# Kernel optimization log

Measured on AMD Instinct MI355X. Metric: run time of the kernel, lower is better.

Reference implementation:

```python
import jax, jax.numpy as jnp
import numpy as np

B, S, E, H = 4, 2048, 1024, 16
D = E // H  # d_k = 64
NEG = -1000000000.0  # matches torch masked_fill constant


def setup_inputs() -> dict:
    rk = jax.random.key(0)
    kq, kk, kv, km = jax.random.split(rk, 4)
    query = jax.random.normal(kq, (B, S, E), dtype=jnp.float32)
    key = jax.random.normal(kk, (B, S, E), dtype=jnp.float32)
    value = jax.random.normal(kv, (B, S, E), dtype=jnp.float32)
    mask = jax.random.randint(km, (B, S, S), 0, 2, dtype=jnp.int32)
    return {"query": query, "key": key, "value": value, "mask": mask}


def _split_heads(x):
    # (B, S, E) -> (B, H, S, D)
    return x.reshape(B, S, H, D).transpose(0, 2, 1, 3)


def reference(query, key, value, mask):
    q = _split_heads(query)
    k = _split_heads(key)
    v = _split_heads(value)
    scale = np.float32(1.0 / np.sqrt(D))
    scores = jnp.einsum('bhqd,bhkd->bhqk', q, k) * scale  # (B,H,S,S)
    scores = jnp.where(mask[:, None, :, :] == 0, jnp.float32(NEG), scores)
    weights = jax.nn.softmax(scores, axis=-1)
    attn = jnp.einsum('bhqk,bhkd->bhqd', weights, v)  # (B,H,S,D)
    concat = attn.transpose(0, 2, 1, 3).reshape(B, S, E)
    return concat
```

## Files before the change

kernel.cpp:

```cpp
#include <hip/hip_runtime.h>
#include <hip/hip_bf16.h>
#include <math.h>

constexpr int B = 4, S = 2048, E = 1024, H = 16, D = 64;
constexpr float NEGF = -1000000000.0f;

typedef __attribute__((ext_vector_type(8))) short short8;
typedef __attribute__((ext_vector_type(16))) float f32x16;

__device__ inline short f2bf(float x) {
    __hip_bfloat16 h = __float2bfloat16(x);
    return *reinterpret_cast<short*>(&h);
}
__device__ inline unsigned pk(float a, float b) {
    return (unsigned)(unsigned short)f2bf(a) | ((unsigned)(unsigned short)f2bf(b) << 16);
}
__device__ inline void gl_lds16(const void* g, void* l) {
    __builtin_amdgcn_global_load_lds(
        (const __attribute__((address_space(1))) unsigned int*)g,
        (__attribute__((address_space(3))) unsigned int*)l, 16, 0, 0);
}

constexpr size_t WS_Q  = 0;
constexpr size_t WS_K  = 18874368;
constexpr size_t WS_VT = 37748736;
constexpr size_t WS_MB = 56623104;
constexpr size_t WS_NEED = 58720256;

__global__ void cvt_qk(const float* __restrict__ src, char* __restrict__ dst, float scale) {
    int g = blockIdx.x * 256 + threadIdx.x;
    int rowd = g >> 2, qtr = g & 3;
    int b = rowd >> 15, h = (rowd >> 11) & 15, s = rowd & 2047;
    const float* p = src + ((size_t)(b * S + s)) * E + h * 64 + qtr * 16;
    float4 v0 = *(const float4*)(p + 0),  v1 = *(const float4*)(p + 4);
    float4 v2 = *(const float4*)(p + 8),  v3 = *(const float4*)(p + 12);
    uint4 o0, o1;
    o0.x = pk(v0.x * scale, v0.y * scale); o0.y = pk(v0.z * scale, v0.w * scale);
    o0.z = pk(v1.x * scale, v1.y * scale); o0.w = pk(v1.z * scale, v1.w * scale);
    o1.x = pk(v2.x * scale, v2.y * scale); o1.y = pk(v2.z * scale, v2.w * scale);
    o1.z = pk(v3.x * scale, v3.y * scale); o1.w = pk(v3.z * scale, v3.w * scale);
    char* d = dst + (size_t)rowd * 144 + qtr * 32;
    *(uint4*)d = o0; *(uint4*)(d + 16) = o1;
}

__global__ void vtrans(const float* __restrict__ V, char* __restrict__ dst) {
    __shared__ float Vf[64][69];
    int t = threadIdx.x;
    int bh = blockIdx.x >> 5, kt = blockIdx.x & 31;
    int b = bh >> 4, h = bh & 15;
    {
        int r = t >> 2, c4 = (t & 3) * 16;
        const float* p = V + ((size_t)(b * S + kt * 64 + r)) * E + h * 64 + c4;
        float4 a = *(const float4*)(p + 0), bb = *(const float4*)(p + 4);
        float4 c = *(const float4*)(p + 8), dd = *(const float4*)(p + 12);
        *(float4*)&Vf[r][c4 + 0] = a;  *(float4*)&Vf[r][c4 + 4] = bb;
        *(float4*)&Vf[r][c4 + 8] = c;  *(float4*)&Vf[r][c4 + 12] = dd;
    }
    __syncthreads();
    int d = t >> 2, sq = (t & 3) * 16;
    float v[16];
#pragma unroll
    for (int i = 0; i < 16; ++i) v[i] = Vf[sq + i][d];
    uint4 o0, o1;
    o0.x = pk(v[0], v[1]);  o0.y = pk(v[2], v[3]);
    o0.z = pk(v[4], v[5]);  o0.w = pk(v[6], v[7]);
    o1.x = pk(v[8], v[9]);  o1.y = pk(v[10], v[11]);
    o1.z = pk(v[12], v[13]); o1.w = pk(v[14], v[15]);
    char* o = dst + ((size_t)(bh * 32 + kt)) * 9216 + d * 144 + sq * 2;
    *(uint4*)o = o0; *(uint4*)(o + 16) = o1;
}

__global__ void maskbits(const int* __restrict__ M, unsigned long long* __restrict__ Mb) {
    int lane = threadIdx.x & 63;
    int gw = blockIdx.x * 4 + (threadIdx.x >> 6);
#pragma unroll
    for (int r = 0; r < 8; ++r) {
        size_t word = (size_t)gw * 8 + r;
        int m = M[word * 64 + lane];
        unsigned long long bal = __ballot(m != 0);
        if (lane == 0) Mb[word] = bal;
    }
}

__global__ __launch_bounds__(256, 2)
void fa_mfma(const char* __restrict__ ws, const unsigned long long* __restrict__ Mb,
             float* __restrict__ O) {
    __shared__ char smem[55296];
    const int tid = threadIdx.x;
    const int w = tid >> 6, lane = tid & 63;
    const int L5 = lane & 31, h6 = lane >> 5;
    const int sh4 = h6 * 4;
    const int h = blockIdx.x & 15, b = (blockIdx.x >> 4) & 3, qt = blockIdx.x >> 6;
    const int bh = b * 16 + h;
    const int q0w = qt * 256 + w * 64;
    char* const Ps = smem + 18432 + w * 9216;

    const char* Qws = ws + WS_Q;
    const char* Kws = ws + WS_K;
    const char* Vtws = ws + WS_VT;

    {
        const char* qsrc = Qws + ((size_t)bh * S + q0w) * 144;
#pragma unroll
        for (int c = 0; c < 9; ++c)
            gl_lds16(qsrc + c * 1024 + lane * 16, Ps + c * 1024);
    }
    __syncthreads();
    short8 qf[2][4];
#pragma unroll
    for (int nb = 0; nb < 2; ++nb)
#pragma unroll
        for (int ks = 0; ks < 4; ++ks)
            qf[nb][ks] = *(const short8*)(Ps + (nb * 32 + L5) * 144 + ks * 32 + h6 * 16);

    f32x16 acc[2][2];
#pragma unroll
    for (int mb = 0; mb < 2; ++mb)
#pragma unroll
        for (int nb = 0; nb < 2; ++nb) acc[mb][nb] = (f32x16)0.0f;
    float l0 = 0.0f, l1 = 0.0f;

    const int qA = q0w + L5, qB = qA + 32;

    for (int kt = 0; kt < S; kt += 64) {
        const int kti = kt >> 6;
        const unsigned long long mA = Mb[((size_t)b * S + qA) * 32 + kti];
        const unsigned long long mB = Mb[((size_t)b * S + qB) * 32 + kti];

        __syncthreads();
        {
            const char* ksrc = Kws + ((size_t)bh * S + kt) * 144;
            const char* vsrc = Vtws + ((size_t)bh * 32 + kti) * 9216;
#pragma unroll
            for (int c = 0; c < 5; ++c) {
                int idx = c * 4 + w;
                if (idx < 18) {
                    int off = idx * 1024;
                    const char* g = (off < 9216) ? (ksrc + off) : (vsrc + off - 9216);
                    gl_lds16(g + lane * 16, smem + off);
                }
            }
        }
        __syncthreads();

#pragma unroll
        for (int mb = 0; mb < 2; ++mb) {
            short8 kf[4];
#pragma unroll
            for (int ks = 0; ks < 4; ++ks)
                kf[ks] = *(const short8*)(smem + (mb * 32 + L5) * 144 + ks * 32 + h6 * 16);
            const unsigned wmA = (unsigned)(mA >> (mb * 32)) >> sh4;
            const unsigned wmB = (unsigned)(mB >> (mb * 32)) >> sh4;
#pragma unroll
            for (int nb = 0; nb < 2; ++nb) {
                f32x16 s = (f32x16)0.0f;
#pragma unroll
                for (int ks = 0; ks < 4; ++ks)
                    s = __builtin_amdgcn_mfma_f32_32x32x16_bf16(kf[ks], qf[nb][ks], s, 0, 0, 0);
                const unsigned wm = nb ? wmB : wmA;
                float p[16], lacc = 0.0f;
#pragma unroll
                for (int r = 0; r < 16; ++r) {
                    const int kc = (r & 3) + 8 * (r >> 2);
                    float sv = ((wm >> kc) & 1u) ? s[r] : NEGF;
                    p[r] = __expf(sv);
                    lacc += p[r];
                }
                if (nb) l1 += lacc; else l0 += lacc;
                char* prow = Ps + (nb * 32 + L5) * 144 + mb * 64 + h6 * 8;
#pragma unroll
                for (int g4 = 0; g4 < 4; ++g4) {
                    short4 t;
                    t.x = f2bf(p[4 * g4 + 0]); t.y = f2bf(p[4 * g4 + 1]);
                    t.z = f2bf(p[4 * g4 + 2]); t.w = f2bf(p[4 * g4 + 3]);
                    *(short4*)(prow + g4 * 16) = t;
                }
            }
        }

        __builtin_amdgcn_s_waitcnt(0xc07f);

        short8 pf[2][4];
#pragma unroll
        for (int nb = 0; nb < 2; ++nb)
#pragma unroll
            for (int ks = 0; ks < 4; ++ks)
                pf[nb][ks] = *(const short8*)(Ps + (nb * 32 + L5) * 144 + ks * 32 + h6 * 16);
#pragma unroll
        for (int mb = 0; mb < 2; ++mb) {
            short8 vf[4];
#pragma unroll
            for (int ks = 0; ks < 4; ++ks)
                vf[ks] = *(const short8*)(smem + 9216 + (mb * 32 + L5) * 144 + ks * 32 + h6 * 16);
#pragma unroll
            for (int nb = 0; nb < 2; ++nb)
#pragma unroll
                for (int ks = 0; ks < 4; ++ks)
                    acc[mb][nb] = __builtin_amdgcn_mfma_f32_32x32x16_bf16(vf[ks], pf[nb][ks], acc[mb][nb], 0, 0, 0);
        }
    }

    l0 += __shfl_xor(l0, 32);
    l1 += __shfl_xor(l1, 32);
    const float inv[2] = {1.0f / l0, 1.0f / l1};
    __syncthreads();
#pragma unroll
    for (int nb = 0; nb < 2; ++nb) {
#pragma unroll
        for (int mb = 0; mb < 2; ++mb)
#pragma unroll
            for (int g4 = 0; g4 < 4; ++g4) {
                float4 t;
                t.x = acc[mb][nb][g4 * 4 + 0] * inv[nb];
                t.y = acc[mb][nb][g4 * 4 + 1] * inv[nb];
                t.z = acc[mb][nb][g4 * 4 + 2] * inv[nb];
                t.w = acc[mb][nb][g4 * 4 + 3] * inv[nb];
                *(float4*)(Ps + (L5 * 68 + mb * 32 + g4 * 8 + h6 * 4) * 4) = t;
            }
        __builtin_amdgcn_s_waitcnt(0xc07f);
        const int r16 = lane >> 4, dc = lane & 15;
#pragma unroll
        for (int i = 0; i < 8; ++i) {
            const int row = i * 4 + r16;
            float4 t = *(const float4*)(Ps + (row * 68 + dc * 4) * 4);
            *(float4*)(O + ((size_t)b * S + q0w + nb * 32 + row) * E + h * 64 + dc * 4) = t;
        }
        __builtin_amdgcn_s_waitcnt(0xc07f);
    }
}

constexpr int QT = 64, KT = 64, LD = D + 4;
constexpr float SCALE = 0.125f;
__global__ __launch_bounds__(256, 3)
void fa_fp32(const float* __restrict__ Q, const float* __restrict__ K,
             const float* __restrict__ V, const int* __restrict__ M,
             float* __restrict__ Out)
{
    __shared__ float Qs[QT][LD];
    __shared__ float Vs[KT][LD];
    __shared__ float KPs[KT][LD];
    const int tid = threadIdx.x, tx = tid & 15, ty = tid >> 4;
    const int bid = blockIdx.x;
    const int h = bid % H, b = (bid / H) % B, qt = bid / (H * B);
    const int q0 = qt * QT;
    {
        const int col = tx * 4;
#pragma unroll
        for (int i = 0; i < 4; ++i) {
            const int row = ty + i * 16;
            *(float4*)&Qs[row][col] = *(const float4*)&Q[((size_t)(b * S + q0 + row)) * E + h * D + col];
        }
    }
    const int qr0 = ty * 4, d0 = tx * 4;
    float acc[4][4] = {};
    float m_i[4], l_i[4];
#pragma unroll
    for (int j = 0; j < 4; ++j) { m_i[j] = -INFINITY; l_i[j] = 0.0f; }
    for (int kt = 0; kt < S; kt += KT) {
        __syncthreads();
        {
            const int col = tx * 4;
#pragma unroll
            for (int i = 0; i < 4; ++i) {
                const int row = ty + i * 16;
                const size_t g = ((size_t)(b * S + kt + row)) * E + h * D + col;
                *(float4*)&KPs[row][col] = *(const float4*)&K[g];
                *(float4*)&Vs[row][col] = *(const float4*)&V[g];
            }
        }
        __syncthreads();
        float s[4][4] = {};
#pragma unroll
        for (int d = 0; d < D; d += 4) {
            float4 a[4], bb[4];
#pragma unroll
            for (int j = 0; j < 4; ++j) a[j] = *(const float4*)&Qs[qr0 + j][d];
#pragma unroll
            for (int i = 0; i < 4; ++i) bb[i] = *(const float4*)&KPs[tx + 16 * i][d];
#pragma unroll
            for (int j = 0; j < 4; ++j)
#pragma unroll
                for (int i = 0; i < 4; ++i)
                    s[j][i] += a[j].x * bb[i].x + a[j].y * bb[i].y + a[j].z * bb[i].z + a[j].w * bb[i].w;
        }
#pragma unroll
        for (int j = 0; j < 4; ++j) {
            const int* mrow = &M[((size_t)b * S + (q0 + qr0 + j)) * S + kt];
#pragma unroll
            for (int i = 0; i < 4; ++i) {
                const int mk = mrow[tx + 16 * i];
                s[j][i] = mk ? s[j][i] * SCALE : NEGF;
            }
        }
#pragma unroll
        for (int j = 0; j < 4; ++j) {
            float tm = fmaxf(fmaxf(s[j][0], s[j][1]), fmaxf(s[j][2], s[j][3]));
#pragma unroll
            for (int off = 8; off; off >>= 1) tm = fmaxf(tm, __shfl_xor(tm, off, 16));
            const float nm = fmaxf(m_i[j], tm);
            const float alpha = __expf(m_i[j] - nm);
            m_i[j] = nm;
            float rs = 0.0f;
#pragma unroll
            for (int i = 0; i < 4; ++i) { const float p = __expf(s[j][i] - nm); s[j][i] = p; rs += p; }
#pragma unroll
            for (int off = 8; off; off >>= 1) rs += __shfl_xor(rs, off, 16);
            l_i[j] = l_i[j] * alpha + rs;
#pragma unroll
            for (int dd = 0; dd < 4; ++dd) acc[j][dd] *= alpha;
        }
        __syncthreads();
#pragma unroll
        for (int j = 0; j < 4; ++j)
#pragma unroll
            for (int i = 0; i < 4; ++i) KPs[qr0 + j][tx + 16 * i] = s[j][i];
        __syncthreads();
#pragma unroll 4
        for (int kk = 0; kk < KT; kk += 4) {
            float4 p[4], vv[4];
#pragma unroll
            for (int j = 0; j < 4; ++j) p[j] = *(const float4*)&KPs[qr0 + j][kk];
#pragma unroll
            for (int u = 0; u < 4; ++u) vv[u] = *(const float4*)&Vs[kk + u][d0];
#pragma unroll
            for (int j = 0; j < 4; ++j) {
                acc[j][0] += p[j].x * vv[0].x + p[j].y * vv[1].x + p[j].z * vv[2].x + p[j].w * vv[3].x;
                acc[j][1] += p[j].x * vv[0].y + p[j].y * vv[1].y + p[j].z * vv[2].y + p[j].w * vv[3].y;
                acc[j][2] += p[j].x * vv[0].z + p[j].y * vv[1].z + p[j].z * vv[2].z + p[j].w * vv[3].z;
                acc[j][3] += p[j].x * vv[0].w + p[j].y * vv[1].w + p[j].z * vv[2].w + p[j].w * vv[3].w;
            }
        }
    }
#pragma unroll
    for (int j = 0; j < 4; ++j) {
        const float iv = 1.0f / l_i[j];
        float4 r;
        r.x = acc[j][0] * iv; r.y = acc[j][1] * iv; r.z = acc[j][2] * iv; r.w = acc[j][3] * iv;
        *(float4*)&Out[((size_t)(b * S + q0 + qr0 + j)) * E + h * D + d0] = r;
    }
}

extern "C" void kernel_launch(void* const* d_in, const int* in_sizes, int n_in,
                              void* d_out, int out_size, void* d_ws, size_t ws_size,
                              hipStream_t stream) {
    (void)in_sizes; (void)n_in; (void)out_size;
    const float* q = (const float*)d_in[0];
    const float* k = (const float*)d_in[1];
    const float* v = (const float*)d_in[2];
    const int*   m = (const int*)d_in[3];
    float* out = (float*)d_out;

    if (ws_size >= WS_NEED) {
        char* ws = (char*)d_ws;
        cvt_qk<<<2048, 256, 0, stream>>>(q, ws + WS_Q, 0.125f);
        cvt_qk<<<2048, 256, 0, stream>>>(k, ws + WS_K, 1.0f);
        vtrans<<<2048, 256, 0, stream>>>(v, ws + WS_VT);
        maskbits<<<8192, 256, 0, stream>>>(m, (unsigned long long*)(ws + WS_MB));
        fa_mfma<<<512, 256, 0, stream>>>(ws, (const unsigned long long*)(ws + WS_MB), out);
    } else {
        fa_fp32<<<B * H * (S / QT), 256, 0, stream>>>(q, k, v, m, out);
    }
}
```

Baseline: 309.5 us.

## Merge preprocessing kernels, double-buffer K/V tiles, keep P in registers

Combines the K conversion, V transpose and mask bit-packing into one prep kernel, and drops the separate Q conversion by loading and converting Q inside the attention kernel. The attention loop now double-buffers K/V tiles in LDS, prefetching the next tile while computing the current one, which removes one barrier per iteration. The softmax probabilities are passed to the PV MFMA through cross-lane shuffles instead of an LDS round trip, and exp2 with log2e folded into the K scale replaces expf. LDS use drops so occupancy can rise to 3 blocks per CU, at the cost of more register pressure and a reworked epilogue.

```diff
diff --git a/kernel.cpp b/kernel.cpp
--- a/kernel.cpp
+++ b/kernel.cpp
@@ -4,6 +4,7 @@
 
 constexpr int B = 4, S = 2048, E = 1024, H = 16, D = 64;
 constexpr float NEGF = -1000000000.0f;
+constexpr float KSCALE = 0.125f * 1.44269504f;
 
 typedef __attribute__((ext_vector_type(8))) short short8;
 typedef __attribute__((ext_vector_type(16))) float f32x16;
@@ -21,71 +22,72 @@
         (__attribute__((address_space(3))) unsigned int*)l, 16, 0, 0);
 }
 
-constexpr size_t WS_Q  = 0;
-constexpr size_t WS_K  = 18874368;
-constexpr size_t WS_VT = 37748736;
-constexpr size_t WS_MB = 56623104;
-constexpr size_t WS_NEED = 58720256;
-
-__global__ void cvt_qk(const float* __restrict__ src, char* __restrict__ dst, float scale) {
-    int g = blockIdx.x * 256 + threadIdx.x;
-    int rowd = g >> 2, qtr = g & 3;
-    int b = rowd >> 15, h = (rowd >> 11) & 15, s = rowd & 2047;
-    const float* p = src + ((size_t)(b * S + s)) * E + h * 64 + qtr * 16;
-    float4 v0 = *(const float4*)(p + 0),  v1 = *(const float4*)(p + 4);
-    float4 v2 = *(const float4*)(p + 8),  v3 = *(const float4*)(p + 12);
-    uint4 o0, o1;
-    o0.x = pk(v0.x * scale, v0.y * scale); o0.y = pk(v0.z * scale, v0.w * scale);
-    o0.z = pk(v1.x * scale, v1.y * scale); o0.w = pk(v1.z * scale, v1.w * scale);
-    o1.x = pk(v2.x * scale, v2.y * scale); o1.y = pk(v2.z * scale, v2.w * scale);
-    o1.z = pk(v3.x * scale, v3.y * scale); o1.w = pk(v3.z * scale, v3.w * scale);
-    char* d = dst + (size_t)rowd * 144 + qtr * 32;
-    *(uint4*)d = o0; *(uint4*)(d + 16) = o1;
-}
-
-__global__ void vtrans(const float* __restrict__ V, char* __restrict__ dst) {
+constexpr size_t WS_K  = 0;
+constexpr size_t WS_VT = 18874368;
+constexpr size_t WS_MB = 37748736;
+constexpr size_t WS_NEED = 39845888;
+
+__global__ void prep(const float* __restrict__ K, const float* __restrict__ V,
+                     const int* __restrict__ M, char* __restrict__ ws) {
     __shared__ float Vf[64][69];
-    int t = threadIdx.x;
-    int bh = blockIdx.x >> 5, kt = blockIdx.x & 31;
-    int b = bh >> 4, h = bh & 15;
-    {
-        int r = t >> 2, c4 = (t & 3) * 16;
-        const float* p = V + ((size_t)(b * S + kt * 64 + r)) * E + h * 64 + c4;
-        float4 a = *(const float4*)(p + 0), bb = *(const float4*)(p + 4);
-        float4 c = *(const float4*)(p + 8), dd = *(const float4*)(p + 12);
-        *(float4*)&Vf[r][c4 + 0] = a;  *(float4*)&Vf[r][c4 + 4] = bb;
-        *(float4*)&Vf[r][c4 + 8] = c;  *(float4*)&Vf[r][c4 + 12] = dd;
-    }
-    __syncthreads();
-    int d = t >> 2, sq = (t & 3) * 16;
-    float v[16];
-#pragma unroll
-    for (int i = 0; i < 16; ++i) v[i] = Vf[sq + i][d];
-    uint4 o0, o1;
-    o0.x = pk(v[0], v[1]);  o0.y = pk(v[2], v[3]);
-    o0.z = pk(v[4], v[5]);  o0.w = pk(v[6], v[7]);
-    o1.x = pk(v[8], v[9]);  o1.y = pk(v[10], v[11]);
-    o1.z = pk(v[12], v[13]); o1.w = pk(v[14], v[15]);
-    char* o = dst + ((size_t)(bh * 32 + kt)) * 9216 + d * 144 + sq * 2;
-    *(uint4*)o = o0; *(uint4*)(o + 16) = o1;
-}
-
-__global__ void maskbits(const int* __restrict__ M, unsigned long long* __restrict__ Mb) {
-    int lane = threadIdx.x & 63;
-    int gw = blockIdx.x * 4 + (threadIdx.x >> 6);
-#pragma unroll
-    for (int r = 0; r < 8; ++r) {
-        size_t word = (size_t)gw * 8 + r;
-        int m = M[word * 64 + lane];
-        unsigned long long bal = __ballot(m != 0);
-        if (lane == 0) Mb[word] = bal;
-    }
-}
-
-__global__ __launch_bounds__(256, 2)
-void fa_mfma(const char* __restrict__ ws, const unsigned long long* __restrict__ Mb,
-             float* __restrict__ O) {
-    __shared__ char smem[55296];
+    const int bid = blockIdx.x, tid = threadIdx.x;
+    if (bid < 2048) {
+        int g = bid * 256 + tid;
+        int rowd = g >> 2, qtr = g & 3;
+        int b = rowd >> 15, h = (rowd >> 11) & 15, s = rowd & 2047;
+        const float* p = K + ((size_t)(b * S + s)) * E + h * 64 + qtr * 16;
+        float4 v0 = *(const float4*)(p + 0),  v1 = *(const float4*)(p + 4);
+        float4 v2 = *(const float4*)(p + 8),  v3 = *(const float4*)(p + 12);
+        uint4 o0, o1;
+        o0.x = pk(v0.x * KSCALE, v0.y * KSCALE); o0.y = pk(v0.z * KSCALE, v0.w * KSCALE);
+        o0.z = pk(v1.x * KSCALE, v1.y * KSCALE); o0.w = pk(v1.z * KSCALE, v1.w * KSCALE);
+        o1.x = pk(v2.x * KSCALE, v2.y * KSCALE); o1.y = pk(v2.z * KSCALE, v2.w * KSCALE);
+        o1.z = pk(v3.x * KSCALE, v3.y * KSCALE); o1.w = pk(v3.z * KSCALE, v3.w * KSCALE);
+        char* d = ws + WS_K + (size_t)rowd * 144 + qtr * 32;
+        *(uint4*)d = o0; *(uint4*)(d + 16) = o1;
+    } else if (bid < 4096) {
+        int blk = bid - 2048;
+        int bh = blk >> 5, kt = blk & 31;
+        int b = bh >> 4, h = bh & 15;
+        {
+            int r = tid >> 2, c4 = (tid & 3) * 16;
+            const float* p = V + ((size_t)(b * S + kt * 64 + r)) * E + h * 64 + c4;
+            float4 a = *(const float4*)(p + 0), bb = *(const float4*)(p + 4);
+            float4 c = *(const float4*)(p + 8), dd = *(const float4*)(p + 12);
+            *(float4*)&Vf[r][c4 + 0] = a;  *(float4*)&Vf[r][c4 + 4] = bb;
+            *(float4*)&Vf[r][c4 + 8] = c;  *(float4*)&Vf[r][c4 + 12] = dd;
+        }
+        __syncthreads();
+        int d = tid >> 2, sq = (tid & 3) * 16;
+        float v[16];
+#pragma unroll
+        for (int i = 0; i < 16; ++i) v[i] = Vf[sq + i][d];
+        uint4 o0, o1;
+        o0.x = pk(v[0], v[1]);   o0.y = pk(v[2], v[3]);
+        o0.z = pk(v[4], v[5]);   o0.w = pk(v[6], v[7]);
+        o1.x = pk(v[8], v[9]);   o1.y = pk(v[10], v[11]);
+        o1.z = pk(v[12], v[13]); o1.w = pk(v[14], v[15]);
+        char* o = ws + WS_VT + ((size_t)(bh * 32 + kt)) * 9216 + d * 144 + sq * 2;
+        *(uint4*)o = o0; *(uint4*)(o + 16) = o1;
+    } else {
+        int blk = bid - 4096;
+        int lane = tid & 63;
+        int wv = blk * 4 + (tid >> 6);
+        unsigned long long* Mb = (unsigned long long*)(ws + WS_MB);
+#pragma unroll 4
+        for (int r = 0; r < 32; ++r) {
+            size_t word = (size_t)wv * 32 + r;
+            int m = M[word * 64 + lane];
+            unsigned long long bal = __ballot(m != 0);
+            if (lane == 0) Mb[word] = bal;
+        }
+    }
+}
+
+__global__ __launch_bounds__(256, 3)
+void fa_mfma(const float* __restrict__ Q, const char* __restrict__ ws,
+             const unsigned long long* __restrict__ Mb, float* __restrict__ O) {
+    __shared__ char smem[36864];
     const int tid = threadIdx.x;
     const int w = tid >> 6, lane = tid & 63;
     const int L5 = lane & 31, h6 = lane >> 5;
@@ -93,25 +95,24 @@
     const int h = blockIdx.x & 15, b = (blockIdx.x >> 4) & 3, qt = blockIdx.x >> 6;
     const int bh = b * 16 + h;
     const int q0w = qt * 256 + w * 64;
-    char* const Ps = smem + 18432 + w * 9216;
-
-    const char* Qws = ws + WS_Q;
-    const char* Kws = ws + WS_K;
+
+    const char* Kws  = ws + WS_K;
     const char* Vtws = ws + WS_VT;
 
-    {
-        const char* qsrc = Qws + ((size_t)bh * S + q0w) * 144;
-#pragma unroll
-        for (int c = 0; c < 9; ++c)
-            gl_lds16(qsrc + c * 1024 + lane * 16, Ps + c * 1024);
-    }
-    __syncthreads();
     short8 qf[2][4];
 #pragma unroll
     for (int nb = 0; nb < 2; ++nb)
 #pragma unroll
-        for (int ks = 0; ks < 4; ++ks)
-            qf[nb][ks] = *(const short8*)(Ps + (nb * 32 + L5) * 144 + ks * 32 + h6 * 16);
+        for (int ks = 0; ks < 4; ++ks) {
+            const float* qp = Q + ((size_t)(b * S + q0w + nb * 32 + L5)) * E
+                                + h * 64 + ks * 16 + h6 * 8;
+            float4 a = *(const float4*)qp;
+            float4 c = *(const float4*)(qp + 4);
+            uint4 u;
+            u.x = pk(a.x, a.y); u.y = pk(a.z, a.w);
+            u.z = pk(c.x, c.y); u.w = pk(c.z, c.w);
+            qf[nb][ks] = *(short8*)&u;
+        }
 
     f32x16 acc[2][2];
 #pragma unroll
@@ -119,38 +120,55 @@
 #pragma unroll
         for (int nb = 0; nb < 2; ++nb) acc[mb][nb] = (f32x16)0.0f;
     float l0 = 0.0f, l1 = 0.0f;
-
     const int qA = q0w + L5, qB = qA + 32;
 
-    for (int kt = 0; kt < S; kt += 64) {
-        const int kti = kt >> 6;
-        const unsigned long long mA = Mb[((size_t)b * S + qA) * 32 + kti];
-        const unsigned long long mB = Mb[((size_t)b * S + qB) * 32 + kti];
-
-        __syncthreads();
-        {
-            const char* ksrc = Kws + ((size_t)bh * S + kt) * 144;
-            const char* vsrc = Vtws + ((size_t)bh * 32 + kti) * 9216;
+    {
+        const char* ksrc = Kws + ((size_t)bh * S) * 144;
+        const char* vsrc = Vtws + ((size_t)bh * 32) * 9216;
+#pragma unroll
+        for (int c = 0; c < 5; ++c) {
+            int idx = c * 4 + w;
+            if (idx < 18) {
+                int off = idx * 1024;
+                const char* g = (off < 9216) ? (ksrc + off) : (vsrc + off - 9216);
+                gl_lds16(g + lane * 16, smem + off);
+            }
+        }
+    }
+
+    for (int ti = 0; ti < 32; ++ti) {
+        __syncthreads();
+
+        if (ti + 1 < 32) {
+            const char* ksrc = Kws + ((size_t)bh * S + (ti + 1) * 64) * 144;
+            const char* vsrc = Vtws + ((size_t)(bh * 32 + ti + 1)) * 9216;
+            char* dst = smem + ((ti + 1) & 1) * 18432;
 #pragma unroll
             for (int c = 0; c < 5; ++c) {
                 int idx = c * 4 + w;
                 if (idx < 18) {
                     int off = idx * 1024;
                     const char* g = (off < 9216) ? (ksrc + off) : (vsrc + off - 9216);
-                    gl_lds16(g + lane * 16, smem + off);
+                    gl_lds16(g + lane * 16, dst + off);
                 }
             }
         }
-        __syncthreads();
-
-#pragma unroll
-        for (int mb = 0; mb < 2; ++mb) {
+        const unsigned long long mA = Mb[((size_t)b * S + qA) * 32 + ti];
+        const unsigned long long mB = Mb[((size_t)b * S + qB) * 32 + ti];
+
+        const char* Ks = smem + (ti & 1) * 18432;
+        const char* Vt = Ks + 9216;
+
+#pragma unroll
+        for (int mbK = 0; mbK < 2; ++mbK) {
             short8 kf[4];
 #pragma unroll
             for (int ks = 0; ks < 4; ++ks)
-                kf[ks] = *(const short8*)(smem + (mb * 32 + L5) * 144 + ks * 32 + h6 * 16);
-            const unsigned wmA = (unsigned)(mA >> (mb * 32)) >> sh4;
-            const unsigned wmB = (unsigned)(mB >> (mb * 32)) >> sh4;
+                kf[ks] = *(const short8*)(Ks + (mbK * 32 + L5) * 144 + ks * 32 + h6 * 16);
+            const unsigned wmA = (unsigned)(mA >> (mbK * 32)) >> sh4;
+            const unsigned wmB = (unsigned)(mB >> (mbK * 32)) >> sh4;
+
+            short8 pf[2][2];
 #pragma unroll
             for (int nb = 0; nb < 2; ++nb) {
                 f32x16 s = (f32x16)0.0f;
@@ -163,70 +181,68 @@
                 for (int r = 0; r < 16; ++r) {
                     const int kc = (r & 3) + 8 * (r >> 2);
                     float sv = ((wm >> kc) & 1u) ? s[r] : NEGF;
-                    p[r] = __expf(sv);
+                    p[r] = __builtin_amdgcn_exp2f(sv);
                     lacc += p[r];
                 }
                 if (nb) l1 += lacc; else l0 += lacc;
-                char* prow = Ps + (nb * 32 + L5) * 144 + mb * 64 + h6 * 8;
-#pragma unroll
-                for (int g4 = 0; g4 < 4; ++g4) {
-                    short4 t;
-                    t.x = f2bf(p[4 * g4 + 0]); t.y = f2bf(p[4 * g4 + 1]);
-                    t.z = f2bf(p[4 * g4 + 2]); t.w = f2bf(p[4 * g4 + 3]);
-                    *(short4*)(prow + g4 * 16) = t;
+                unsigned pd[8];
+#pragma unroll
+                for (int i = 0; i < 8; ++i) pd[i] = pk(p[2 * i], p[2 * i + 1]);
+#pragma unroll
+                for (int sub = 0; sub < 2; ++sub) {
+                    const unsigned dA = pd[4 * sub + 0], dB = pd[4 * sub + 1];
+                    const unsigned dC = pd[4 * sub + 2], dD = pd[4 * sub + 3];
+                    const unsigned t0 = h6 ? dA : dC;
+                    const unsigned t1 = h6 ? dB : dD;
+                    const unsigned r0 = (unsigned)__shfl_xor((int)t0, 32, 64);
+                    const unsigned r1 = (unsigned)__shfl_xor((int)t1, 32, 64);
+                    uint4 u;
+                    u.x = h6 ? r0 : dA;  u.y = h6 ? r1 : dB;
+                    u.z = h6 ? dC : r0;  u.w = h6 ? dD : r1;
+                    pf[nb][sub] = *(short8*)&u;
                 }
             }
-        }
-
-        __builtin_amdgcn_s_waitcnt(0xc07f);
-
-        short8 pf[2][4];
-#pragma unroll
-        for (int nb = 0; nb < 2; ++nb)
-#pragma unroll
-            for (int ks = 0; ks < 4; ++ks)
-                pf[nb][ks] = *(const short8*)(Ps + (nb * 32 + L5) * 144 + ks * 32 + h6 * 16);
-#pragma unroll
-        for (int mb = 0; mb < 2; ++mb) {
-            short8 vf[4];
-#pragma unroll
-            for (int ks = 0; ks < 4; ++ks)
-                vf[ks] = *(const short8*)(smem + 9216 + (mb * 32 + L5) * 144 + ks * 32 + h6 * 16);
-#pragma unroll
-            for (int nb = 0; nb < 2; ++nb)
-#pragma unroll
-                for (int ks = 0; ks < 4; ++ks)
-                    acc[mb][nb] = __builtin_amdgcn_mfma_f32_32x32x16_bf16(vf[ks], pf[nb][ks], acc[mb][nb], 0, 0, 0);
-        }
-    }
-
-    l0 += __shfl_xor(l0, 32);
-    l1 += __shfl_xor(l1, 32);
+#pragma unroll
+            for (int mbV = 0; mbV < 2; ++mbV) {
+                short8 vf[2];
+#pragma unroll
+                for (int sub = 0; sub < 2; ++sub)
+                    vf[sub] = *(const short8*)(Vt + (mbV * 32 + L5) * 144
+                                               + (mbK * 2 + sub) * 32 + h6 * 16);
+#pragma unroll
+                for (int nb = 0; nb < 2; ++nb)
+#pragma unroll
+                    for (int sub = 0; sub < 2; ++sub)
+                        acc[mbV][nb] = __builtin_amdgcn_mfma_f32_32x32x16_bf16(
+                            vf[sub], pf[nb][sub], acc[mbV][nb], 0, 0, 0);
+            }
+        }
+    }
+
+    l0 += __shfl_xor(l0, 32, 64);
+    l1 += __shfl_xor(l1, 32, 64);
     const float inv[2] = {1.0f / l0, 1.0f / l1};
     __syncthreads();
-#pragma unroll
-    for (int nb = 0; nb < 2; ++nb) {
-#pragma unroll
-        for (int mb = 0; mb < 2; ++mb)
-#pragma unroll
-            for (int g4 = 0; g4 < 4; ++g4) {
-                float4 t;
-                t.x = acc[mb][nb][g4 * 4 + 0] * inv[nb];
-                t.y = acc[mb][nb][g4 * 4 + 1] * inv[nb];
-                t.z = acc[mb][nb][g4 * 4 + 2] * inv[nb];
-                t.w = acc[mb][nb][g4 * 4 + 3] * inv[nb];
-                *(float4*)(Ps + (L5 * 68 + mb * 32 + g4 * 8 + h6 * 4) * 4) = t;
-            }
-        __builtin_amdgcn_s_waitcnt(0xc07f);
-        const int r16 = lane >> 4, dc = lane & 15;
-#pragma unroll
-        for (int i = 0; i < 8; ++i) {
-            const int row = i * 4 + r16;
-            float4 t = *(const float4*)(Ps + (row * 68 + dc * 4) * 4);
-            *(float4*)(O + ((size_t)b * S + q0w + nb * 32 + row) * E + h * 64 + dc * 4) = t;
-        }
-        __builtin_amdgcn_s_waitcnt(0xc07f);
-    }
+    float* ep = (float*)(smem + w * 4608);
+#pragma unroll
+    for (int nb = 0; nb < 2; ++nb)
+#pragma unroll
+        for (int mb = 0; mb < 2; ++mb) {
+#pragma unroll
+            for (int r = 0; r < 16; ++r) {
+                const int d = (r & 3) + 8 * (r >> 2) + sh4;
+                ep[L5 * 36 + d] = acc[mb][nb][r] * inv[nb];
+            }
+            __builtin_amdgcn_s_waitcnt(0xc07f);
+            const int row = lane >> 1, c = (lane & 1) * 16;
+#pragma unroll
+            for (int i = 0; i < 4; ++i) {
+                float4 t = *(const float4*)&ep[row * 36 + c + 4 * i];
+                *(float4*)(O + ((size_t)(b * S + q0w + nb * 32 + row)) * E
+                             + h * 64 + mb * 32 + c + 4 * i) = t;
+            }
+            __builtin_amdgcn_s_waitcnt(0xc07f);
+        }
 }
 
 constexpr int QT = 64, KT = 64, LD = D + 4;
@@ -352,11 +368,9 @@
 
     if (ws_size >= WS_NEED) {
         char* ws = (char*)d_ws;
-        cvt_qk<<<2048, 256, 0, stream>>>(q, ws + WS_Q, 0.125f);
-        cvt_qk<<<2048, 256, 0, stream>>>(k, ws + WS_K, 1.0f);
-        vtrans<<<2048, 256, 0, stream>>>(v, ws + WS_VT);
-        maskbits<<<8192, 256, 0, stream>>>(m, (unsigned long long*)(ws + WS_MB));
-        fa_mfma<<<512, 256, 0, stream>>>(ws, (const unsigned long long*)(ws + WS_MB), out);
+        prep<<<6144, 256, 0, stream>>>(k, v, m, ws);
+        fa_mfma<<<512, 256, 0, stream>>>(q, ws,
+            (const unsigned long long*)(ws + WS_MB), out);
     } else {
         fa_fp32<<<B * H * (S / QT), 256, 0, stream>>>(q, k, v, m, out);
     }
```

Result: slower. 453.6 us (+46.5%).
